# Optimization experiments

Measured on AMD Instinct MI355X. Metric: run time of the kernel, lower is better.

The kernel has to match this reference:

```python
import jax, jax.numpy as jnp
import numpy as np

DIM = 1024
DIM_HEAD = 64
HEADS = 16
INNER = DIM_HEAD * HEADS
SCALE = 8.0
EPS_LN = 1e-5
EPS_L2 = 1e-12


def _layernorm(x, gamma):
    mu = jnp.mean(x, axis=-1, keepdims=True)
    var = jnp.var(x, axis=-1, keepdims=True)
    return (x - mu) / jnp.sqrt(var + EPS_LN) * gamma  # beta is a zero buffer


def _l2norm(t):
    n = jnp.linalg.norm(t, axis=-1, keepdims=True)
    return t / jnp.maximum(n, EPS_L2)


def setup_inputs() -> dict:
    key = jax.random.key(0)
    ks = jax.random.split(key, 8)
    b, n = 4, 2048
    x = jax.random.normal(ks[0], (b, n, DIM), dtype=jnp.float32)
    context_mask = jax.random.randint(ks[1], (b, n), 0, 2) > 0
    gamma = jnp.ones((DIM,), dtype=jnp.float32)
    wq = jax.random.normal(ks[2], (DIM, INNER), dtype=jnp.float32) * 0.02
    wkv = jax.random.normal(ks[3], (DIM, 2 * INNER), dtype=jnp.float32) * 0.02
    null_kv = jax.random.normal(ks[4], (2, HEADS, 1, DIM_HEAD), dtype=jnp.float32)
    q_scale = jnp.ones((DIM_HEAD,), dtype=jnp.float32)
    k_scale = jnp.ones((DIM_HEAD,), dtype=jnp.float32)
    wo = jax.random.normal(ks[5], (INNER, DIM), dtype=jnp.float32) * 0.02
    return {"x": x, "context_mask": context_mask, "gamma": gamma, "wq": wq,
            "wkv": wkv, "null_kv": null_kv, "q_scale": q_scale,
            "k_scale": k_scale, "wo": wo}


def reference(x, context_mask, gamma, wq, wkv, null_kv, q_scale, k_scale, wo):
    b, n, _ = x.shape
    xn = _layernorm(x, gamma)
    q = xn @ wq                     # [b, n, inner]
    kv = xn @ wkv                   # self-attention: kv_input = x
    k, v = jnp.split(kv, 2, axis=-1)

    def split_heads(t):
        return t.reshape(b, n, HEADS, DIM_HEAD).transpose(0, 2, 1, 3)  # b h n d

    q, k, v = map(split_heads, (q, k, v))
    nk = jnp.broadcast_to(null_kv[0][None], (b, HEADS, 1, DIM_HEAD))
    nv = jnp.broadcast_to(null_kv[1][None], (b, HEADS, 1, DIM_HEAD))
    k = jnp.concatenate([nk, k], axis=2)  # b h (n+1) d
    v = jnp.concatenate([nv, v], axis=2)

    q = _l2norm(q) * q_scale
    k = _l2norm(k) * k_scale

    sim = jnp.einsum('bhid,bhjd->bhij', q, k) * SCALE  # b h n (n+1)
    mask = jnp.pad(context_mask, ((0, 0), (1, 0)), constant_values=True)  # null kv always visible
    mask_value = -jnp.finfo(sim.dtype).max
    sim = jnp.where(mask[:, None, None, :], sim, mask_value)

    attn = jax.nn.softmax(sim, axis=-1)
    out = jnp.einsum('bhij,bhjd->bhid', attn, v)
    out = out.transpose(0, 2, 1, 3).reshape(b, n, INNER)
    return out @ wo
```

## Files before the change

### kernel.cpp

```cpp
#include <hip/hip_runtime.h>

typedef unsigned short u16;
typedef unsigned int u32;
typedef unsigned long long u64;
typedef __bf16 bf16x8 __attribute__((ext_vector_type(8)));
typedef float f32x4 __attribute__((ext_vector_type(4)));

#define B_ 4
#define N_ 2048
#define D_ 1024
#define H_ 16
#define DH_ 64
#define NKP_ 2112
#define NKT_ 33

__device__ __forceinline__ float bf2f(u16 u) {
  union { u32 i; float f; } v; v.i = ((u32)u) << 16; return v.f;
}
__device__ __forceinline__ u16 f2bf(float f) {
  union { float f; u32 i; } v; v.f = f;
  u32 r = v.i + 0x7fffu + ((v.i >> 16) & 1u);
  return (u16)(r >> 16);
}
__device__ __forceinline__ u32 cvtpk(float a, float b) {
  u32 r;
  asm("v_cvt_pk_bf16_f32 %0, %1, %2" : "=v"(r) : "v"(a), "v"(b));
  return r;
}
__device__ __forceinline__ void load_lds16(const void* g, void* l) {
  __builtin_amdgcn_global_load_lds((const __attribute__((address_space(1))) void*)g,
                                   (__attribute__((address_space(3))) void*)l, 16, 0, 0);
}

__global__ __launch_bounds__(256) void ln_kernel(const float* __restrict__ x,
                                                 const float* __restrict__ gamma,
                                                 u16* __restrict__ xn) {
  int row = blockIdx.x;
  int tid = threadIdx.x, lane = tid & 63, wid = tid >> 6;
  const float4 v = ((const float4*)(x + (size_t)row * D_))[tid];
  float s  = v.x + v.y + v.z + v.w;
  float ss = v.x * v.x + v.y * v.y + v.z * v.z + v.w * v.w;
#pragma unroll
  for (int off = 1; off < 64; off <<= 1) {
    s  += __shfl_xor(s,  off, 64);
    ss += __shfl_xor(ss, off, 64);
  }
  __shared__ float rs[4], rss[4];
  if (lane == 0) { rs[wid] = s; rss[wid] = ss; }
  __syncthreads();
  float S  = rs[0] + rs[1] + rs[2] + rs[3];
  float SS = rss[0] + rss[1] + rss[2] + rss[3];
  float mean = S * (1.0f / D_);
  float var  = SS * (1.0f / D_) - mean * mean;
  float inv  = rsqrtf(var + 1e-5f);
  const float4 g = ((const float4*)gamma)[tid];
  ushort4 o;
  o.x = f2bf((v.x - mean) * inv * g.x);
  o.y = f2bf((v.y - mean) * inv * g.y);
  o.z = f2bf((v.z - mean) * inv * g.z);
  o.w = f2bf((v.w - mean) * inv * g.w);
  *(ushort4*)(xn + (size_t)row * D_ + tid * 4) = o;
}

__global__ __launch_bounds__(256) void wt_kernel(const float* __restrict__ W,
                                                 u16* __restrict__ WT,
                                                 int K, int N) {
  __shared__ float t[32][33];
  int tiles_n = N >> 5;
  int tk = blockIdx.x / tiles_n, tn = blockIdx.x % tiles_n;
  int tx = threadIdx.x & 31, ty = threadIdx.x >> 5;
  int k0 = tk << 5, n0 = tn << 5;
#pragma unroll
  for (int i = 0; i < 4; ++i)
    t[ty + i * 8][tx] = W[(size_t)(k0 + ty + i * 8) * N + n0 + tx];
  __syncthreads();
#pragma unroll
  for (int i = 0; i < 4; ++i)
    WT[(size_t)(n0 + ty + i * 8) * K + k0 + tx] = f2bf(t[tx][ty + i * 8]);
}

__global__ __launch_bounds__(256) void prep_kernel(const int* __restrict__ mask,
                                                   const float* __restrict__ qs,
                                                   const float* __restrict__ ksc,
                                                   const float* __restrict__ null_kv,
                                                   u16* __restrict__ Kb,
                                                   u16* __restrict__ Vt,
                                                   float* __restrict__ cb) {
  __shared__ int cnts[4];
  int bh = blockIdx.x, h = bh & 15;
  int tid = threadIdx.x, lane = tid & 63, wid = tid >> 6;
  if (wid == 0) {
    float kv = null_kv[h * 64 + lane];
    float ss = kv * kv;
#pragma unroll
    for (int off = 1; off < 64; off <<= 1) ss += __shfl_xor(ss, off, 64);
    float inv = 1.0f / fmaxf(sqrtf(ss), 1e-12f);
    Kb[((size_t)bh * NKP_ + 2048) * 64 + lane] = f2bf(kv * inv * ksc[lane]);
    Vt[((size_t)bh * 64 + lane) * NKP_ + 2048] = f2bf(null_kv[1024 + h * 64 + lane]);
  }
  for (int i = tid; i < 63 * 64; i += 256) {
    int r = i >> 6, c = i & 63;
    Kb[((size_t)bh * NKP_ + 2049 + r) * 64 + c] = 0;
  }
  for (int i = tid; i < 64 * 63; i += 256) {
    int d = i / 63, c = i % 63;
    Vt[((size_t)bh * 64 + d) * NKP_ + 2049 + c] = 0;
  }
  if (bh == 0) {
    if (tid < 4) cnts[tid] = 0;
    __syncthreads();
    int c0 = 0, c1 = 0, c2 = 0, c3 = 0;
    for (int i = tid; i < B_ * N_; i += 256) {
      int z = (mask[i] == 0);
      int b = i >> 11;
      if (b == 0) c0 += z; else if (b == 1) c1 += z; else if (b == 2) c2 += z; else c3 += z;
    }
    atomicAdd(&cnts[0], c0); atomicAdd(&cnts[1], c1);
    atomicAdd(&cnts[2], c2); atomicAdd(&cnts[3], c3);
    __syncthreads();
    if (tid == 0) {
      float mw = 0.f;
      for (int i = 0; i < DH_; ++i) mw = fmaxf(mw, fabsf(qs[i] * ksc[i]));
      float cbias = -8.0f * mw * 1.4426950408889634f;
      cb[0] = cbias;
      float e = __builtin_amdgcn_exp2f(cbias);
#pragma unroll
      for (int b = 0; b < 4; ++b) cb[1 + b] = (float)(cnts[b] + 63) * e;
    }
  }
}

#define GEMM_BODY(A, Bt)                                                       \
  int tid = threadIdx.x, lane = tid & 63, wid = tid >> 6;                      \
  int m0 = blockIdx.x * 128, n0 = blockIdx.y * 128;                            \
  int wm = (wid >> 1) * 64, wn = (wid & 1) * 64;                               \
  int sr = lane >> 3;                                                          \
  int scz = ((lane & 7) ^ (lane >> 3)) * 8;       \
  int la = lane & 15, lk = (lane >> 4) * 8;                                    \
  int swz = (la & 7) * 8;                                   \
  f32x4 acc[4][4] = {};                                                        \
  for (int kt = 0; kt < 16; ++kt) {                                            \
    int k0_ = kt * 64;                                                         \
    __syncthreads();                                                           \
    _Pragma("unroll")                                                          \
    for (int i_ = 0; i_ < 4; ++i_) {                                           \
      int r_ = i_ * 32 + wid * 8;                                              \
      load_lds16(A + (size_t)(m0 + r_ + sr) * 1024 + k0_ + scz, &a_sm[r_ * 64]); \
      load_lds16(Bt + (size_t)(n0 + r_ + sr) * 1024 + k0_ + scz, &b_sm[r_ * 64]); \
    }                                                                          \
    __syncthreads();                                                           \
    _Pragma("unroll")                                                          \
    for (int s = 0; s < 2; ++s) {                                              \
      bf16x8 af[4], bfr[4];                                                    \
      _Pragma("unroll")                                                        \
      for (int mf = 0; mf < 4; ++mf)                                           \
        af[mf] = *(const bf16x8*)&a_sm[(wm + mf * 16 + la) * 64 + ((s * 32 + lk) ^ swz)]; \
      _Pragma("unroll")                                                        \
      for (int nf = 0; nf < 4; ++nf)                                           \
        bfr[nf] = *(const bf16x8*)&b_sm[(wn + nf * 16 + la) * 64 + ((s * 32 + lk) ^ swz)]; \
      _Pragma("unroll")                                                        \
      for (int mf = 0; mf < 4; ++mf)                                           \
        _Pragma("unroll")                                                      \
        for (int nf = 0; nf < 4; ++nf)                                         \
          acc[mf][nf] = __builtin_amdgcn_mfma_f32_16x16x32_bf16(af[mf], bfr[nf], acc[mf][nf], 0, 0, 0); \
    }                                                                          \
  }                                                                            \
  int crow = (lane >> 4) * 4, ccol = lane & 15;

__global__ __launch_bounds__(256) void gemm_qkv(const u16* __restrict__ A,
                                                const u16* __restrict__ Bt,
                                                u16* __restrict__ Qo,
                                                u16* __restrict__ Kb,
                                                u16* __restrict__ Vt,
                                                const float* __restrict__ qs,
                                                const float* __restrict__ ksc,
                                                const int* __restrict__ Mask) {
  __shared__ __attribute__((aligned(16))) u16 sm[2 * 128 * 64];
  u16* a_sm = sm;
  u16* b_sm = sm + 128 * 64;
  GEMM_BODY(A, Bt)

  int by = blockIdx.y;
  if (by < 8) {
    float qsv[4];
#pragma unroll
    for (int nf = 0; nf < 4; ++nf) qsv[nf] = qs[nf * 16 + ccol];
#pragma unroll
    for (int mf = 0; mf < 4; ++mf) {
      float invr[4];
#pragma unroll
      for (int r = 0; r < 4; ++r) {
        float ss = 0.f;
#pragma unroll
        for (int nf = 0; nf < 4; ++nf) ss += acc[mf][nf][r] * acc[mf][nf][r];
#pragma unroll
        for (int off = 1; off < 16; off <<= 1) ss += __shfl_xor(ss, off, 64);
        invr[r] = 1.0f / fmaxf(sqrtf(ss), 1e-12f);
      }
#pragma unroll
      for (int nf = 0; nf < 4; ++nf) {
        int rr = m0 + wm + mf * 16 + crow;
        int cc = n0 + wn + nf * 16 + ccol;
#pragma unroll
        for (int r = 0; r < 4; ++r)
          Qo[(size_t)(rr + r) * 1024 + cc] = f2bf(acc[mf][nf][r] * invr[r] * qsv[nf]);
      }
    }
    return;
  }

  int rr0 = m0 + wm;
  int b = rr0 >> 11;
  int seq0 = rr0 & 2047;
  const int* mrow = Mask + b * N_ + seq0;
  if (by < 16) {
    int h = (by - 8) * 2 + (wn >> 6);
    float kscv[4];
#pragma unroll
    for (int nf = 0; nf < 4; ++nf) kscv[nf] = ksc[nf * 16 + ccol];
    u16* kb = Kb + ((size_t)(b * 16 + h) * NKP_) * 64;
#pragma unroll
    for (int mf = 0; mf < 4; ++mf) {
      float invr[4]; int mvv[4];
#pragma unroll
      for (int r = 0; r < 4; ++r) {
        float ss = 0.f;
#pragma unroll
        for (int nf = 0; nf < 4; ++nf) ss += acc[mf][nf][r] * acc[mf][nf][r];
#pragma unroll
        for (int off = 1; off < 16; off <<= 1) ss += __shfl_xor(ss, off, 64);
        invr[r] = 1.0f / fmaxf(sqrtf(ss), 1e-12f);
        mvv[r] = mrow[mf * 16 + crow + r];
      }
#pragma unroll
      for (int nf = 0; nf < 4; ++nf)
#pragma unroll
        for (int r = 0; r < 4; ++r)
          kb[(size_t)(seq0 + mf * 16 + crow + r) * 64 + nf * 16 + ccol] =
              f2bf(mvv[r] ? acc[mf][nf][r] * invr[r] * kscv[nf] : 0.f);
    }
  } else {
    int h = (by - 16) * 2 + (wn >> 6);
    __syncthreads();
    u16* tw = sm + wid * 4096;
#pragma unroll
    for (int mf = 0; mf < 4; ++mf) {
      int mvv[4];
#pragma unroll
      for (int r = 0; r < 4; ++r) mvv[r] = mrow[mf * 16 + crow + r];
#pragma unroll
      for (int nf = 0; nf < 4; ++nf) {
        int row = nf * 16 + ccol;
#pragma unroll
        for (int r = 0; r < 4; ++r)
          tw[row * 64 + ((mf * 16 + crow + r) ^ ((row & 7) * 8))] =
              f2bf(mvv[r] ? acc[mf][nf][r] : 0.f);
      }
    }
    u16* vb = Vt + ((size_t)(b * 16 + h) * 64) * NKP_;
    int dr = lane >> 3, kc = (lane & 7) * 8;
#pragma unroll
    for (int i = 0; i < 8; ++i) {
      int d = i * 8 + dr;
      bf16x8 vv = *(const bf16x8*)&tw[d * 64 + (kc ^ ((d & 7) * 8))];
      *(bf16x8*)(vb + (size_t)d * NKP_ + seq0 + kc) = vv;
    }
  }
}

__global__ __launch_bounds__(256) void gemm_out(const u16* __restrict__ A,
                                                const u16* __restrict__ Bt,
                                                float* __restrict__ C) {
  __shared__ __attribute__((aligned(16))) u16 sm[2 * 128 * 64];
  u16* a_sm = sm;
  u16* b_sm = sm + 128 * 64;
  GEMM_BODY(A, Bt)
#pragma unroll
  for (int mf = 0; mf < 4; ++mf)
#pragma unroll
    for (int nf = 0; nf < 4; ++nf) {
      int rr = m0 + wm + mf * 16 + crow;
      int cc = n0 + wn + nf * 16 + ccol;
#pragma unroll
      for (int r = 0; r < 4; ++r) C[(size_t)(rr + r) * 1024 + cc] = acc[mf][nf][r];
    }
}

__global__ __launch_bounds__(512) void attn_kernel(const u16* __restrict__ Q,
                                                   const u16* __restrict__ Kb,
                                                   const u16* __restrict__ Vt,
                                                   const float* __restrict__ cb,
                                                   u16* __restrict__ O) {
  __shared__ __attribute__((aligned(16))) u16 k_sm[2][64 * 64];
  __shared__ __attribute__((aligned(16))) u16 v_sm[2][64 * 64];
  __shared__ __attribute__((aligned(16))) u16 p_sm[8][32 * 64];
  int tid = threadIdx.x, lane = tid & 63, wid = tid >> 6;
  int bh = blockIdx.x, b = bh >> 4, h = bh & 15;
  int q0 = blockIdx.y * 256 + wid * 32;
  int la = lane & 15, lk = (lane >> 4) * 8, crow = (lane >> 4) * 4;
  int swz = (la & 7) * 8;
  int sr = lane >> 3;
  int scz = ((lane & 7) ^ (lane >> 3)) * 8;

  bf16x8 aq[2][2];
#pragma unroll
  for (int qb = 0; qb < 2; ++qb) {
    const u16* qrow = Q + ((size_t)(b * N_) + q0 + qb * 16 + la) * D_ + h * DH_;
#pragma unroll
    for (int s = 0; s < 2; ++s) aq[qb][s] = *(const bf16x8*)(qrow + s * 32 + lk);
  }
  float l[2] = {0.f, 0.f};
  f32x4 o[2][4] = {};
  const u16* Kbh = Kb + (size_t)bh * NKP_ * 64;
  const u16* Vbh = Vt + (size_t)bh * 64 * NKP_;
  const float C1 = 11.541560327111707f;
  const float cbias = cb[0];
  const float lsub = cb[1 + b];

#define STAGE(bb, kt)                                                          \
  do {                                                                         \
    int key0_ = (kt) * 64;                                                     \
    int r_ = wid * 8;                                                          \
    load_lds16(Kbh + (size_t)(key0_ + r_ + sr) * 64 + scz, &k_sm[bb][r_ * 64]); \
    load_lds16(Vbh + (size_t)(r_ + sr) * NKP_ + key0_ + scz, &v_sm[bb][r_ * 64]); \
  } while (0)

  STAGE(0, 0);

#pragma unroll 2
  for (int kt = 0; kt < NKT_; ++kt) {
    int bb = kt & 1;
    __syncthreads();
    if (kt + 1 < NKT_) STAGE(bb ^ 1, kt + 1);

    f32x4 sacc[2][4] = {};
    __builtin_amdgcn_s_setprio(1);
#pragma unroll
    for (int nf = 0; nf < 4; ++nf) {
      bf16x8 bk0 = *(const bf16x8*)&k_sm[bb][(nf * 16 + la) * 64 + (lk ^ swz)];
      bf16x8 bk1 = *(const bf16x8*)&k_sm[bb][(nf * 16 + la) * 64 + ((32 + lk) ^ swz)];
#pragma unroll
      for (int qb = 0; qb < 2; ++qb) {
        sacc[qb][nf] = __builtin_amdgcn_mfma_f32_16x16x32_bf16(bk0, aq[qb][0], sacc[qb][nf], 0, 0, 0);
        sacc[qb][nf] = __builtin_amdgcn_mfma_f32_16x16x32_bf16(bk1, aq[qb][1], sacc[qb][nf], 0, 0, 0);
      }
    }
    __builtin_amdgcn_s_setprio(0);

#pragma unroll
    for (int nf = 0; nf < 4; ++nf) {
      int key = nf * 16 + crow;
#pragma unroll
      for (int qb = 0; qb < 2; ++qb) {
        float p0 = __builtin_amdgcn_exp2f(fmaf(sacc[qb][nf][0], C1, cbias));
        float p1 = __builtin_amdgcn_exp2f(fmaf(sacc[qb][nf][1], C1, cbias));
        float p2 = __builtin_amdgcn_exp2f(fmaf(sacc[qb][nf][2], C1, cbias));
        float p3 = __builtin_amdgcn_exp2f(fmaf(sacc[qb][nf][3], C1, cbias));
        l[qb] += (p0 + p1) + (p2 + p3);
        uint2 pw;
        pw.x = cvtpk(p0, p1);
        pw.y = cvtpk(p2, p3);
        *(uint2*)&p_sm[wid][(qb * 16 + la) * 64 + (key ^ swz)] = pw;
      }
    }

    __builtin_amdgcn_s_setprio(1);
#pragma unroll
    for (int s = 0; s < 2; ++s) {
      bf16x8 bv[4];
#pragma unroll
      for (int dt = 0; dt < 4; ++dt)
        bv[dt] = *(const bf16x8*)&v_sm[bb][(dt * 16 + la) * 64 + ((s * 32 + lk) ^ swz)];
#pragma unroll
      for (int qb = 0; qb < 2; ++qb) {
        bf16x8 ap = *(const bf16x8*)&p_sm[wid][(qb * 16 + la) * 64 + ((s * 32 + lk) ^ swz)];
#pragma unroll
        for (int dt = 0; dt < 4; ++dt)
          o[qb][dt] = __builtin_amdgcn_mfma_f32_16x16x32_bf16(ap, bv[dt], o[qb][dt], 0, 0, 0);
      }
    }
    __builtin_amdgcn_s_setprio(0);
  }
#undef STAGE

#pragma unroll
  for (int qb = 0; qb < 2; ++qb) {
    l[qb] += __shfl_xor(l[qb], 16, 64);
    l[qb] += __shfl_xor(l[qb], 32, 64);
#pragma unroll
    for (int r = 0; r < 4; ++r) {
      float lq = __shfl(l[qb], crow + r, 64) - lsub;
      float inv = 1.0f / lq;
      int n = q0 + qb * 16 + crow + r;
      u16* ob = O + ((size_t)(b * N_) + n) * D_ + h * DH_;
#pragma unroll
      for (int dt = 0; dt < 4; ++dt) ob[dt * 16 + la] = f2bf(o[qb][dt][r] * inv);
    }
  }
}

extern "C" void kernel_launch(void* const* d_in, const int* in_sizes, int n_in,
                              void* d_out, int out_size, void* d_ws, size_t ws_size,
                              hipStream_t stream) {
  (void)in_sizes; (void)n_in; (void)out_size; (void)ws_size;
  const float* x     = (const float*)d_in[0];
  const int*   mask  = (const int*)d_in[1];
  const float* gamma = (const float*)d_in[2];
  const float* wq    = (const float*)d_in[3];
  const float* wkv   = (const float*)d_in[4];
  const float* nkv   = (const float*)d_in[5];
  const float* qs    = (const float*)d_in[6];
  const float* ksc   = (const float*)d_in[7];
  const float* wo    = (const float*)d_in[8];

  char* ws   = (char*)d_ws;
  u16* xn    = (u16*)(ws);
  u16* wqkvT = (u16*)(ws + (16ull << 20));
  u16* wkvT  = wqkvT + 1024 * 1024;
  u16* woT   = (u16*)(ws + (22ull << 20));
  u16* Kb    = (u16*)(ws + (24ull << 20));
  u16* Vt    = (u16*)(ws + (41ull << 20));
  float* cb  = (float*)(ws + (58ull << 20));
  u16* q_tmp = (u16*)d_out;
  u16* attn_out = xn;

  ln_kernel<<<B_ * N_, 256, 0, stream>>>(x, gamma, xn);
  wt_kernel<<<(1024 / 32) * (1024 / 32), 256, 0, stream>>>(wq, wqkvT, 1024, 1024);
  wt_kernel<<<(1024 / 32) * (2048 / 32), 256, 0, stream>>>(wkv, wkvT, 1024, 2048);
  wt_kernel<<<(1024 / 32) * (1024 / 32), 256, 0, stream>>>(wo, woT, 1024, 1024);
  prep_kernel<<<64, 256, 0, stream>>>(mask, qs, ksc, nkv, Kb, Vt, cb);
  gemm_qkv<<<dim3(64, 24), 256, 0, stream>>>(xn, wqkvT, q_tmp, Kb, Vt, qs, ksc, mask);
  attn_kernel<<<dim3(64, 8), 512, 0, stream>>>(q_tmp, Kb, Vt, cb, attn_out);
  gemm_out<<<dim3(64, 8), 256, 0, stream>>>(attn_out, woT, (float*)d_out);
}
```

Measured before the change: 211.4 us.

## Rewrite QKV GEMM with 256x256 tiles, 512 threads and double-buffered LDS

```diff
diff --git a/kernel.cpp b/kernel.cpp
--- a/kernel.cpp
+++ b/kernel.cpp
@@ -130,14 +130,168 @@
   }
 }
 
+__global__ __launch_bounds__(512, 1) void gemm_qkv(const u16* __restrict__ A,
+                                                   const u16* __restrict__ Bt,
+                                                   u16* __restrict__ Qo,
+                                                   u16* __restrict__ Kb,
+                                                   u16* __restrict__ Vt,
+                                                   const float* __restrict__ qs,
+                                                   const float* __restrict__ ksc,
+                                                   const int* __restrict__ Mask) {
+  __shared__ __attribute__((aligned(16))) u16 dsm[65536];
+  int tid = threadIdx.x, lane = tid & 63, wid = tid >> 6;
+  int wr = wid >> 2, wc = wid & 3;
+  int m0 = blockIdx.x * 256, n0 = blockIdx.y * 256;
+  int wm = wr * 128, wn = wc * 64;
+  int la = lane & 15, hi = lane >> 4, crow = hi * 4;
+  int sr = lane >> 3;
+  int scz = ((lane & 7) ^ (lane >> 3)) * 8;
+  f32x4 acc[8][4] = {};
+
+#define QSTAGE(buf, kt)                                                        \
+  do {                                                                         \
+    int k0_ = (kt) * 64;                                                       \
+    u16* ab_ = dsm + (buf) * 32768;                                            \
+    _Pragma("unroll")                                                          \
+    for (int r4 = 0; r4 < 4; ++r4) {                                           \
+      int r_ = r4 * 64 + wid * 8;                   \
+      load_lds16(A  + (size_t)(m0 + r_ + sr) * 1024 + k0_ + scz, ab_ + r_ * 64); \
+      load_lds16(Bt + (size_t)(n0 + r_ + sr) * 1024 + k0_ + scz, ab_ + 16384 + r_ * 64); \
+    }                                                                          \
+  } while (0)
+
+  QSTAGE(0, 0);
+
+  for (int kt = 0; kt < 16; ++kt) {
+    int buf = kt & 1;
+    __syncthreads();
+    if (kt + 1 < 16) QSTAGE(buf ^ 1, kt + 1);
+    const u16* a_l = dsm + buf * 32768;
+    const u16* b_l = a_l + 16384;
+    __builtin_amdgcn_s_setprio(1);
+#pragma unroll
+    for (int s = 0; s < 2; ++s) {
+      int slotbase = s * 4 + hi;
+      bf16x8 bfr[4];
+#pragma unroll
+      for (int nf = 0; nf < 4; ++nf)
+        bfr[nf] = *(const bf16x8*)&b_l[(wn + nf * 16 + la) * 64 + ((slotbase ^ (la & 7)) * 8)];
+#pragma unroll
+      for (int mf = 0; mf < 8; ++mf) {
+        bf16x8 af = *(const bf16x8*)&a_l[(wm + mf * 16 + la) * 64 + ((slotbase ^ (la & 7)) * 8)];
+#pragma unroll
+        for (int nf = 0; nf < 4; ++nf)
+          acc[mf][nf] = __builtin_amdgcn_mfma_f32_16x16x32_bf16(af, bfr[nf], acc[mf][nf], 0, 0, 0);
+      }
+    }
+    __builtin_amdgcn_s_setprio(0);
+  }
+#undef QSTAGE
+
+  int by = blockIdx.y, ccol = la;
+  if (by < 4) {
+    float qsv[4];
+#pragma unroll
+    for (int nf = 0; nf < 4; ++nf) qsv[nf] = qs[nf * 16 + ccol];
+#pragma unroll
+    for (int mf = 0; mf < 8; ++mf) {
+      float invr[4];
+#pragma unroll
+      for (int r = 0; r < 4; ++r) {
+        float ss = 0.f;
+#pragma unroll
+        for (int nf = 0; nf < 4; ++nf) ss += acc[mf][nf][r] * acc[mf][nf][r];
+#pragma unroll
+        for (int off = 1; off < 16; off <<= 1) ss += __shfl_xor(ss, off, 64);
+        invr[r] = 1.0f / fmaxf(sqrtf(ss), 1e-12f);
+      }
+#pragma unroll
+      for (int nf = 0; nf < 4; ++nf) {
+        int rr = m0 + wm + mf * 16 + crow;
+        int cc = by * 256 + wn + nf * 16 + ccol;
+#pragma unroll
+        for (int r = 0; r < 4; ++r)
+          Qo[(size_t)(rr + r) * 1024 + cc] = f2bf(acc[mf][nf][r] * invr[r] * qsv[nf]);
+      }
+    }
+    return;
+  }
+
+  int rr0 = m0 + wm;
+  int b = rr0 >> 11;
+  int seq0 = rr0 & 2047;
+  const int* mrow = Mask + b * N_ + seq0;
+  if (by < 8) {
+    int h = (by - 4) * 4 + wc;
+    float kscv[4];
+#pragma unroll
+    for (int nf = 0; nf < 4; ++nf) kscv[nf] = ksc[nf * 16 + ccol];
+    u16* kb = Kb + ((size_t)(b * 16 + h) * NKP_) * 64;
+#pragma unroll
+    for (int mf = 0; mf < 8; ++mf) {
+      float invr[4]; int mvv[4];
+#pragma unroll
+      for (int r = 0; r < 4; ++r) {
+        float ss = 0.f;
+#pragma unroll
+        for (int nf = 0; nf < 4; ++nf) ss += acc[mf][nf][r] * acc[mf][nf][r];
+#pragma unroll
+        for (int off = 1; off < 16; off <<= 1) ss += __shfl_xor(ss, off, 64);
+        invr[r] = 1.0f / fmaxf(sqrtf(ss), 1e-12f);
+        mvv[r] = mrow[mf * 16 + crow + r];
+      }
+#pragma unroll
+      for (int nf = 0; nf < 4; ++nf)
+#pragma unroll
+        for (int r = 0; r < 4; ++r)
+          kb[(size_t)(seq0 + mf * 16 + crow + r) * 64 + nf * 16 + ccol] =
+              f2bf(mvv[r] ? acc[mf][nf][r] * invr[r] * kscv[nf] : 0.f);
+    }
+  } else {
+    int h = (by - 8) * 4 + wc;
+    __syncthreads();
+    u16* tw = dsm + wid * 8192;
+#pragma unroll
+    for (int mf = 0; mf < 8; ++mf) {
+      int mvv[4];
+#pragma unroll
+      for (int r = 0; r < 4; ++r) mvv[r] = mrow[mf * 16 + crow + r];
+#pragma unroll
+      for (int nf = 0; nf < 4; ++nf) {
+        int d = nf * 16 + ccol;
+#pragma unroll
+        for (int r = 0; r < 4; ++r) {
+          int key = mf * 16 + crow + r;
+          tw[d * 128 + ((((key >> 3) ^ (d & 7)) << 3) | (key & 7))] =
+              f2bf(mvv[r] ? acc[mf][nf][r] : 0.f);
+        }
+      }
+    }
+    u16* vb = Vt + ((size_t)(b * 16 + h) * 64) * NKP_ + seq0 + wm - wm;
+    vb = Vt + ((size_t)(b * 16 + h) * 64) * NKP_;
+    int key0 = seq0;
+    int dr = lane >> 3, kc8 = (lane & 7);
+#pragma unroll
+    for (int j = 0; j < 8; ++j) {
+      int d = j * 8 + dr;
+#pragma unroll
+      for (int half = 0; half < 2; ++half) {
+        int kslot = kc8 + half * 8;
+        bf16x8 vv = *(const bf16x8*)&tw[d * 128 + (((kslot ^ (d & 7)) & 15) * 8)];
+        *(bf16x8*)(vb + (size_t)d * NKP_ + key0 + kslot * 8) = vv;
+      }
+    }
+  }
+}
+
 #define GEMM_BODY(A, Bt)                                                       \
   int tid = threadIdx.x, lane = tid & 63, wid = tid >> 6;                      \
   int m0 = blockIdx.x * 128, n0 = blockIdx.y * 128;                            \
   int wm = (wid >> 1) * 64, wn = (wid & 1) * 64;                               \
   int sr = lane >> 3;                                                          \
-  int scz = ((lane & 7) ^ (lane >> 3)) * 8;       \
+  int scz = ((lane & 7) ^ (lane >> 3)) * 8;                                    \
   int la = lane & 15, lk = (lane >> 4) * 8;                                    \
-  int swz = (la & 7) * 8;                                   \
+  int swz = (la & 7) * 8;                                                      \
   f32x4 acc[4][4] = {};                                                        \
   for (int kt = 0; kt < 16; ++kt) {                                            \
     int k0_ = kt * 64;                                                         \
@@ -167,107 +321,6 @@
   }                                                                            \
   int crow = (lane >> 4) * 4, ccol = lane & 15;
 
-__global__ __launch_bounds__(256) void gemm_qkv(const u16* __restrict__ A,
-                                                const u16* __restrict__ Bt,
-                                                u16* __restrict__ Qo,
-                                                u16* __restrict__ Kb,
-                                                u16* __restrict__ Vt,
-                                                const float* __restrict__ qs,
-                                                const float* __restrict__ ksc,
-                                                const int* __restrict__ Mask) {
-  __shared__ __attribute__((aligned(16))) u16 sm[2 * 128 * 64];
-  u16* a_sm = sm;
-  u16* b_sm = sm + 128 * 64;
-  GEMM_BODY(A, Bt)
-
-  int by = blockIdx.y;
-  if (by < 8) {
-    float qsv[4];
-#pragma unroll
-    for (int nf = 0; nf < 4; ++nf) qsv[nf] = qs[nf * 16 + ccol];
-#pragma unroll
-    for (int mf = 0; mf < 4; ++mf) {
-      float invr[4];
-#pragma unroll
-      for (int r = 0; r < 4; ++r) {
-        float ss = 0.f;
-#pragma unroll
-        for (int nf = 0; nf < 4; ++nf) ss += acc[mf][nf][r] * acc[mf][nf][r];
-#pragma unroll
-        for (int off = 1; off < 16; off <<= 1) ss += __shfl_xor(ss, off, 64);
-        invr[r] = 1.0f / fmaxf(sqrtf(ss), 1e-12f);
-      }
-#pragma unroll
-      for (int nf = 0; nf < 4; ++nf) {
-        int rr = m0 + wm + mf * 16 + crow;
-        int cc = n0 + wn + nf * 16 + ccol;
-#pragma unroll
-        for (int r = 0; r < 4; ++r)
-          Qo[(size_t)(rr + r) * 1024 + cc] = f2bf(acc[mf][nf][r] * invr[r] * qsv[nf]);
-      }
-    }
-    return;
-  }
-
-  int rr0 = m0 + wm;
-  int b = rr0 >> 11;
-  int seq0 = rr0 & 2047;
-  const int* mrow = Mask + b * N_ + seq0;
-  if (by < 16) {
-    int h = (by - 8) * 2 + (wn >> 6);
-    float kscv[4];
-#pragma unroll
-    for (int nf = 0; nf < 4; ++nf) kscv[nf] = ksc[nf * 16 + ccol];
-    u16* kb = Kb + ((size_t)(b * 16 + h) * NKP_) * 64;
-#pragma unroll
-    for (int mf = 0; mf < 4; ++mf) {
-      float invr[4]; int mvv[4];
-#pragma unroll
-      for (int r = 0; r < 4; ++r) {
-        float ss = 0.f;
-#pragma unroll
-        for (int nf = 0; nf < 4; ++nf) ss += acc[mf][nf][r] * acc[mf][nf][r];
-#pragma unroll
-        for (int off = 1; off < 16; off <<= 1) ss += __shfl_xor(ss, off, 64);
-        invr[r] = 1.0f / fmaxf(sqrtf(ss), 1e-12f);
-        mvv[r] = mrow[mf * 16 + crow + r];
-      }
-#pragma unroll
-      for (int nf = 0; nf < 4; ++nf)
-#pragma unroll
-        for (int r = 0; r < 4; ++r)
-          kb[(size_t)(seq0 + mf * 16 + crow + r) * 64 + nf * 16 + ccol] =
-              f2bf(mvv[r] ? acc[mf][nf][r] * invr[r] * kscv[nf] : 0.f);
-    }
-  } else {
-    int h = (by - 16) * 2 + (wn >> 6);
-    __syncthreads();
-    u16* tw = sm + wid * 4096;
-#pragma unroll
-    for (int mf = 0; mf < 4; ++mf) {
-      int mvv[4];
-#pragma unroll
-      for (int r = 0; r < 4; ++r) mvv[r] = mrow[mf * 16 + crow + r];
-#pragma unroll
-      for (int nf = 0; nf < 4; ++nf) {
-        int row = nf * 16 + ccol;
-#pragma unroll
-        for (int r = 0; r < 4; ++r)
-          tw[row * 64 + ((mf * 16 + crow + r) ^ ((row & 7) * 8))] =
-              f2bf(mvv[r] ? acc[mf][nf][r] : 0.f);
-      }
-    }
-    u16* vb = Vt + ((size_t)(b * 16 + h) * 64) * NKP_;
-    int dr = lane >> 3, kc = (lane & 7) * 8;
-#pragma unroll
-    for (int i = 0; i < 8; ++i) {
-      int d = i * 8 + dr;
-      bf16x8 vv = *(const bf16x8*)&tw[d * 64 + (kc ^ ((d & 7) * 8))];
-      *(bf16x8*)(vb + (size_t)d * NKP_ + seq0 + kc) = vv;
-    }
-  }
-}
-
 __global__ __launch_bounds__(256) void gemm_out(const u16* __restrict__ A,
                                                 const u16* __restrict__ Bt,
                                                 float* __restrict__ C) {
@@ -429,7 +482,7 @@
   wt_kernel<<<(1024 / 32) * (2048 / 32), 256, 0, stream>>>(wkv, wkvT, 1024, 2048);
   wt_kernel<<<(1024 / 32) * (1024 / 32), 256, 0, stream>>>(wo, woT, 1024, 1024);
   prep_kernel<<<64, 256, 0, stream>>>(mask, qs, ksc, nkv, Kb, Vt, cb);
-  gemm_qkv<<<dim3(64, 24), 256, 0, stream>>>(xn, wqkvT, q_tmp, Kb, Vt, qs, ksc, mask);
+  gemm_qkv<<<dim3(32, 12), 512, 0, stream>>>(xn, wqkvT, q_tmp, Kb, Vt, qs, ksc, mask);
   attn_kernel<<<dim3(64, 8), 512, 0, stream>>>(q_tmp, Kb, Vt, cb, attn_out);
   gemm_out<<<dim3(64, 8), 256, 0, stream>>>(attn_out, woT, (float*)d_out);
 }
```

After: 204.1 us. 1.04x faster.
